# Kernel optimization log

Measured on AMD Instinct MI355X. Metric: run time of the kernel, lower is better.

Reference implementation:

```python
import jax, jax.numpy as jnp
import numpy as np

B, T, D, H = 4, 2048, 512, 8
DH = D // H  # 64
EPS = 1e-5


def setup_inputs() -> dict:
    key = jax.random.key(0)
    ks = jax.random.split(key, 12)
    s = lambda k, shp, fan: jax.random.normal(k, shp, jnp.float32) * (fan ** -0.5)
    return {
        "x": jax.random.normal(ks[0], (B, T, D), jnp.float32),
        "ln1_g": jnp.ones((D,), jnp.float32),
        "ln1_b": jnp.zeros((D,), jnp.float32),
        "Wq": s(ks[1], (H, D, DH), D),  # per-head bias-free projections
        "Wk": s(ks[2], (H, D, DH), D),
        "Wv": s(ks[3], (H, D, DH), D),
        "Wproj": s(ks[4], (D, D), D),
        "bproj": jnp.zeros((D,), jnp.float32),
        "W1": s(ks[5], (D, 4 * D), D),
        "b1": jnp.zeros((4 * D,), jnp.float32),
        "W2": s(ks[6], (4 * D, D), 4 * D),
        "b2": jnp.zeros((D,), jnp.float32),
    }


def _layernorm(x, g, b):
    m = jnp.mean(x, axis=-1, keepdims=True)
    v = jnp.var(x, axis=-1, keepdims=True)
    return (x - m) * jax.lax.rsqrt(v + EPS) * g + b


def reference(x, ln1_g, ln1_b, Wq, Wk, Wv, Wproj, bproj, W1, b1, W2, b2):
    b, t, c = x.shape
    scale = c ** -0.5  # source scales by input channel dim, not head_size
    causal = jnp.tril(jnp.ones((t, t), bool))  # [T,T]

    # --- attention sublayer (pre-norm with ln1) ---
    h = _layernorm(x, ln1_g, ln1_b)
    q = jnp.einsum('btd,hde->bhte', h, Wq)
    k = jnp.einsum('btd,hde->bhte', h, Wk)
    v = jnp.einsum('btd,hde->bhte', h, Wv)
    scores = jnp.einsum('bhte,bhse->bhts', q, k) * scale  # [B,H,T,T]
    scores = jnp.where(causal, scores, -jnp.inf)
    att = jax.nn.softmax(scores, axis=-1)  # dropout = identity at inference
    o = jnp.einsum('bhts,bhse->bthe', att, v).reshape(b, t, c)  # concat heads
    sa = o @ Wproj + bproj
    x = x + sa

    # --- FFN sublayer (source reuses ln1, faithful) ---
    h2 = _layernorm(x, ln1_g, ln1_b)
    ff = jax.nn.relu(h2 @ W1 + b1) @ W2 + b2
    return x + ff
```

## Files before the change

### kernel.cpp

```cpp
#include <hip/hip_runtime.h>
#include <math.h>

#define B_ 4
#define T_ 2048
#define D_ 512
#define H_ 8
#define DH_ 64
#define BT_ 8192
#define FF_ 2048
#define EPS_ 1e-5f
#define SCALE_ 0.04419417382415922f
#define SC2_ 0.06375861151f
#define NEGINF_ -1e30f

typedef short b16x8 __attribute__((ext_vector_type(8)));
typedef short b16x4 __attribute__((ext_vector_type(4)));
typedef float f32x4 __attribute__((ext_vector_type(4)));

#define MFMA16(a, b, c) __builtin_amdgcn_mfma_f32_16x16x32_bf16(a, b, c, 0, 0, 0)
#define MFMA16K16(a, b, c) __builtin_amdgcn_mfma_f32_16x16x16bf16_1k(a, b, c, 0, 0, 0)

#define GLL16(gp, lp) \
    __builtin_amdgcn_global_load_lds((const __attribute__((address_space(1))) void*)(gp), \
                                     (__attribute__((address_space(3))) void*)(lp), 16, 0, 0)

#if __has_builtin(__builtin_amdgcn_exp2f)
#define EXP2F(x) __builtin_amdgcn_exp2f(x)
#else
#define EXP2F(x) exp2f(x)
#endif

static __device__ inline short f2bf(float f) {
    unsigned int u = __builtin_bit_cast(unsigned int, f);
    unsigned int r = (u + 0x7fffu + ((u >> 16) & 1u)) >> 16;
    return (short)r;
}
static __device__ inline short f2bf_trunc(float f) {
    return (short)(__builtin_bit_cast(unsigned int, f) >> 16);
}
static __device__ inline float bf2f(short s) {
    return __builtin_bit_cast(float, ((unsigned int)(unsigned short)s) << 16);
}

__global__ __launch_bounds__(256) void prologue_kernel(
        const float* __restrict__ Wq, const float* __restrict__ Wk,
        const float* __restrict__ Wv, const float* __restrict__ Wp,
        const float* __restrict__ W1, const float* __restrict__ W2,
        short* __restrict__ wqkv, short* __restrict__ wpt,
        short* __restrict__ w1t, short* __restrict__ w2t,
        const float* __restrict__ X, const float* __restrict__ G,
        const float* __restrict__ Bb, short* __restrict__ Y)
{
    __shared__ float tile[32][33];
    int idx = blockIdx.x;
    if (idx >= 3072) {
        int tid = threadIdx.y * 32 + threadIdx.x;
        int wave = tid >> 6, t = tid & 63;
        int row = (idx - 3072) * 4 + wave;
        const float* xr = X + (size_t)row * D_;
        float4 v0 = *(const float4*)(xr + t * 4);
        float4 v1 = *(const float4*)(xr + 256 + t * 4);
        float sum = v0.x + v0.y + v0.z + v0.w + v1.x + v1.y + v1.z + v1.w;
        float ssq = v0.x*v0.x + v0.y*v0.y + v0.z*v0.z + v0.w*v0.w
                  + v1.x*v1.x + v1.y*v1.y + v1.z*v1.z + v1.w*v1.w;
        #pragma unroll
        for (int off = 32; off > 0; off >>= 1) {
            sum += __shfl_down(sum, off);
            ssq += __shfl_down(ssq, off);
        }
        sum = __shfl(sum, 0);
        ssq = __shfl(ssq, 0);
        float mean = sum * (1.0f / D_);
        float var  = ssq * (1.0f / D_) - mean * mean;
        float rstd = rsqrtf(var + EPS_);
        float4 g0 = *(const float4*)(G + t * 4);
        float4 g1 = *(const float4*)(G + 256 + t * 4);
        float4 b0 = *(const float4*)(Bb + t * 4);
        float4 b1 = *(const float4*)(Bb + 256 + t * 4);
        short4 o0, o1;
        o0.x = f2bf((v0.x - mean) * rstd * g0.x + b0.x);
        o0.y = f2bf((v0.y - mean) * rstd * g0.y + b0.y);
        o0.z = f2bf((v0.z - mean) * rstd * g0.z + b0.z);
        o0.w = f2bf((v0.w - mean) * rstd * g0.w + b0.w);
        o1.x = f2bf((v1.x - mean) * rstd * g1.x + b1.x);
        o1.y = f2bf((v1.y - mean) * rstd * g1.y + b1.y);
        o1.z = f2bf((v1.z - mean) * rstd * g1.z + b1.z);
        o1.w = f2bf((v1.w - mean) * rstd * g1.w + b1.w);
        short* yr = Y + (size_t)row * D_;
        *(short4*)(yr + t * 4)       = o0;
        *(short4*)(yr + 256 + t * 4) = o1;
        return;
    }
    const float* src; short* dst; int R, C, tx0, ty0;
    if (idx < 768) {
        int w = idx >> 8, rem = idx & 255;
        int hh = rem >> 5, t = rem & 31;
        const float* base = (w == 0) ? Wq : ((w == 1) ? Wk : Wv);
        src = base + hh * (D_ * DH_);
        dst = wqkv + w * (512 * 512) + hh * (DH_ * D_);
        R = 512; C = 64; tx0 = (t & 1) * 32; ty0 = (t >> 1) * 32;
    } else if (idx < 1024) {
        int t = idx - 768;
        src = Wp; dst = wpt; R = 512; C = 512;
        tx0 = (t & 15) * 32; ty0 = (t >> 4) * 32;
    } else if (idx < 2048) {
        int t = idx - 1024;
        src = W1; dst = w1t; R = 512; C = 2048;
        tx0 = (t & 63) * 32; ty0 = (t >> 6) * 32;
    } else {
        int t = idx - 2048;
        src = W2; dst = w2t; R = 2048; C = 512;
        tx0 = (t & 15) * 32; ty0 = (t >> 4) * 32;
    }
    int tx = threadIdx.x, ty = threadIdx.y;
    #pragma unroll
    for (int i = 0; i < 32; i += 8)
        tile[ty + i][tx] = src[(size_t)(ty0 + ty + i) * C + tx0 + tx];
    __syncthreads();
    #pragma unroll
    for (int i = 0; i < 32; i += 8)
        dst[(size_t)(tx0 + ty + i) * R + ty0 + tx] = f2bf(tile[tx][ty + i]);
}

__global__ __launch_bounds__(256) void ln_bf16_kernel(const short* __restrict__ X,
        const float* __restrict__ G, const float* __restrict__ Bb,
        short* __restrict__ Y)
{
    int wave = threadIdx.x >> 6, t = threadIdx.x & 63;
    int row = blockIdx.x * 4 + wave;
    const short* xr = X + (size_t)row * D_ + t * 8;
    b16x8 xv = *(const b16x8*)xr;
    float v[8];
    float sum = 0.0f, ssq = 0.0f;
    #pragma unroll
    for (int e = 0; e < 8; ++e) {
        v[e] = bf2f(xv[e]);
        sum += v[e];
        ssq += v[e] * v[e];
    }
    #pragma unroll
    for (int off = 32; off > 0; off >>= 1) {
        sum += __shfl_down(sum, off);
        ssq += __shfl_down(ssq, off);
    }
    sum = __shfl(sum, 0);
    ssq = __shfl(ssq, 0);
    float mean = sum * (1.0f / D_);
    float var  = ssq * (1.0f / D_) - mean * mean;
    float rstd = rsqrtf(var + EPS_);

    float4 g0 = *(const float4*)(G + t * 8);
    float4 g1 = *(const float4*)(G + t * 8 + 4);
    float4 b0 = *(const float4*)(Bb + t * 8);
    float4 b1 = *(const float4*)(Bb + t * 8 + 4);
    float gg[8] = {g0.x, g0.y, g0.z, g0.w, g1.x, g1.y, g1.z, g1.w};
    float bb[8] = {b0.x, b0.y, b0.z, b0.w, b1.x, b1.y, b1.z, b1.w};
    b16x8 o;
    #pragma unroll
    for (int e = 0; e < 8; ++e)
        o[e] = f2bf((v[e] - mean) * rstd * gg[e] + bb[e]);
    *(b16x8*)(Y + (size_t)row * D_ + t * 8) = o;
}

__global__ __launch_bounds__(512, 2) void mm256_kernel(const short* __restrict__ A,
        const short* __restrict__ Bt, void* __restrict__ C,
        const float* __restrict__ bias, int relu, int N, int K)
{
    __shared__ short As[2][256 * 64];
    __shared__ short Bs[2][256 * 64];
    const int tid = threadIdx.x;
    const int wave = tid >> 6, lane = tid & 63;
    const int quad = lane >> 4, l15 = lane & 15;
    const int m0 = blockIdx.x * 256, n0 = blockIdx.y * 256;
    const int mw = (wave & 1) * 128, nw = (wave >> 1) * 64;

#define STAGE_M256(bufi, kk) \
    { \
        for (int r = 0; r < 4; ++r) { \
            int c = r * 512 + tid; \
            int row = c >> 3, seg = (c & 7) ^ (row & 7); \
            GLL16(A + (size_t)(m0 + row) * K + (kk) + seg * 8, \
                  As[bufi] + (size_t)(r * 512 + wave * 64) * 8); \
            GLL16(Bt + (size_t)(n0 + row) * K + (kk) + seg * 8, \
                  Bs[bufi] + (size_t)(r * 512 + wave * 64) * 8); \
        } \
    }

    f32x4 acc[8][4];
    #pragma unroll
    for (int i = 0; i < 8; ++i)
        #pragma unroll
        for (int j = 0; j < 4; ++j)
            acc[i][j] = (f32x4){0.f, 0.f, 0.f, 0.f};

    const int NT = K >> 6;
    STAGE_M256(0, 0);
    int buf = 0;
    for (int t = 0; t < NT; ++t) {
        __syncthreads();
        if (t + 1 < NT) STAGE_M256(buf ^ 1, (t + 1) * 64);
        #pragma unroll
        for (int kb = 0; kb < 2; ++kb) {
            b16x8 af[8], bf[4];
            #pragma unroll
            for (int i = 0; i < 8; ++i) {
                int row = mw + i * 16 + l15;
                af[i] = *(const b16x8*)(As[buf] + row * 64 + (((kb * 4 + quad) ^ (row & 7)) * 8));
            }
            #pragma unroll
            for (int j = 0; j < 4; ++j) {
                int row = nw + j * 16 + l15;
                bf[j] = *(const b16x8*)(Bs[buf] + row * 64 + (((kb * 4 + quad) ^ (row & 7)) * 8));
            }
            #pragma unroll
            for (int i = 0; i < 8; ++i)
                #pragma unroll
                for (int j = 0; j < 4; ++j)
                    acc[i][j] = MFMA16(af[i], bf[j], acc[i][j]);
        }
        buf ^= 1;
    }
#undef STAGE_M256

    #pragma unroll
    for (int i = 0; i < 8; ++i) {
        #pragma unroll
        for (int r = 0; r < 4; ++r) {
            size_t row = (size_t)(m0 + mw + i * 16 + quad * 4 + r);
            #pragma unroll
            for (int j = 0; j < 4; ++j) {
                int col = n0 + nw + j * 16 + l15;
                float v = acc[i][j][r];
                if (bias)  v += bias[col];
                if (relu)  v = fmaxf(v, 0.0f);
                ((short*)C)[row * N + col] = f2bf(v);
            }
        }
    }
}

__global__ __launch_bounds__(256) void mm6464_kernel(const short* __restrict__ A,
        const short* __restrict__ Bt, void* __restrict__ C,
        const float* __restrict__ bias, const void* __restrict__ resid,
        int M, int N, int K, int relu, int out_bf16, int resid_bf16)
{
    __shared__ short As[2][64 * 64];
    __shared__ short Bs[2][64 * 64];
    const int tid = threadIdx.x;
    const int wave = tid >> 6, lane = tid & 63;
    const int quad = lane >> 4, l15 = lane & 15;
    const int m0 = blockIdx.x * 64, n0 = blockIdx.y * 64;
    const int nw = wave * 16;

#define STAGE_M66(bufi, kk) \
    { \
        for (int r = 0; r < 2; ++r) { \
            int c = r * 256 + tid; \
            int row = c >> 3, seg = (c & 7) ^ (row & 7); \
            GLL16(A + (size_t)(m0 + row) * K + (kk) + seg * 8, \
                  As[bufi] + (size_t)(r * 256 + wave * 64) * 8); \
            GLL16(Bt + (size_t)(n0 + row) * K + (kk) + seg * 8, \
                  Bs[bufi] + (size_t)(r * 256 + wave * 64) * 8); \
        } \
    }

    f32x4 acc[4];
    #pragma unroll
    for (int i = 0; i < 4; ++i) acc[i] = (f32x4){0.f, 0.f, 0.f, 0.f};

    STAGE_M66(0, 0);
    int buf = 0;
    for (int k0 = 0; k0 < K; k0 += 64) {
        __syncthreads();
        if (k0 + 64 < K) STAGE_M66(buf ^ 1, k0 + 64);
        b16x8 af[4][2], bf[2];
        #pragma unroll
        for (int i = 0; i < 4; ++i)
            #pragma unroll
            for (int kb = 0; kb < 2; ++kb) {
                int row = i * 16 + l15;
                af[i][kb] = *(const b16x8*)(As[buf] + row * 64 + (((kb * 4 + quad) ^ (row & 7)) * 8));
            }
        #pragma unroll
        for (int kb = 0; kb < 2; ++kb) {
            int row = nw + l15;
            bf[kb] = *(const b16x8*)(Bs[buf] + row * 64 + (((kb * 4 + quad) ^ (row & 7)) * 8));
        }
        #pragma unroll
        for (int kb = 0; kb < 2; ++kb)
            #pragma unroll
            for (int i = 0; i < 4; ++i)
                acc[i] = MFMA16(af[i][kb], bf[kb], acc[i]);
        buf ^= 1;
    }
#undef STAGE_M66

    #pragma unroll
    for (int i = 0; i < 4; ++i) {
        #pragma unroll
        for (int r = 0; r < 4; ++r) {
            size_t row = (size_t)(m0 + i * 16 + quad * 4 + r);
            int col = n0 + nw + l15;
            float v = acc[i][r];
            if (bias)  v += bias[col];
            if (resid) {
                if (resid_bf16) v += bf2f(((const short*)resid)[row * N + col]);
                else            v += ((const float*)resid)[row * N + col];
            }
            if (relu)  v = fmaxf(v, 0.0f);
            if (out_bf16) ((short*)C)[row * N + col] = f2bf(v);
            else          ((float*)C)[row * N + col] = v;
        }
    }
}

__global__ __launch_bounds__(256) void attn_kernel(const short* __restrict__ qkv,
        short* __restrict__ Opart, float* __restrict__ Ml)
{
    __shared__ short Qs[64 * 72];
    __shared__ short Ks[64 * 64];
    __shared__ short Vt[64 * 64];

    const int tid = threadIdx.x;
    const int wave = tid >> 6, lane = tid & 63;
    const int quad = lane >> 4, l15 = lane & 15;
    const int bh = blockIdx.x;
    const int qi = 31 - (int)blockIdx.y;
    const int split = blockIdx.z;
    const int b = bh >> 3, h = bh & 7;
    const size_t tok0 = (size_t)b * T_;
    const int qrow_rel = wave * 16 + l15;
    const int half = (qi + 1) >> 1;
    const int klo = split ? half : 0;
    const int khi = split ? qi + 1 : half;
    const int pidx = split * 1024 + bh * 32 + qi;
    short* Op = Opart + (size_t)pidx * 4096;
    float* mlp = Ml + (size_t)pidx * 64;

    if (klo >= khi) {
        for (int i = tid; i < 2048; i += 256) ((int*)Op)[i] = 0;
        if (tid < 64) mlp[tid] = 0.0f;
        return;
    }

    #pragma unroll
    for (int r = 0; r < 2; ++r) {
        int c = r * 256 + tid;
        int tk = c >> 3;
        int seg = (c & 7) ^ (tk & 7);
        GLL16(qkv + (tok0 + qi * 64 + tk) * 1536 + h * 64 + seg * 8,
              Qs + (size_t)(r * 256 + wave * 64) * 8);
    }

    float lrow = 0.0f;
    f32x4 ot[4];
    #pragma unroll
    for (int dt = 0; dt < 4; ++dt) ot[dt] = (f32x4){0.f, 0.f, 0.f, 0.f};

    b16x8 qf[2];

    for (int kj = klo; kj < khi; ++kj) {
        __syncthreads();
        #pragma unroll
        for (int r = 0; r < 2; ++r) {
            int c = r * 256 + tid;
            int tk = c >> 3;
            int seg = (c & 7) ^ (tk & 7);
            GLL16(qkv + (tok0 + kj * 64 + tk) * 1536 + 512 + h * 64 + seg * 8,
                  Ks + (size_t)(r * 256 + wave * 64) * 8);
        }
        {
            int s = tid >> 5, tp = tid & 31;
            const short* g0 = qkv + (tok0 + kj * 64 + tp * 2) * 1536 + 1024 + h * 64 + s * 8;
            b16x8 v0 = *(const b16x8*)g0;
            b16x8 v1 = *(const b16x8*)(g0 + 1536);
            int* vo = (int*)Vt;
            int gg = tp >> 1, hlf = tp & 1;
            #pragma unroll
            for (int e = 0; e < 8; ++e) {
                int row = s * 8 + e;
                unsigned int pk = (unsigned int)(unsigned short)v0[e]
                                | ((unsigned int)(unsigned short)v1[e] << 16);
                vo[row * 32 + ((gg ^ (row & 15)) << 1) + hlf] = pk;
            }
        }
        __syncthreads();

        if (kj == klo) {
            #pragma unroll
            for (int kb = 0; kb < 2; ++kb) {
                int row = wave * 16 + l15;
                qf[kb] = *(const b16x8*)(Qs + row * 64 + (((kb * 4 + quad) ^ (row & 7)) * 8));
            }
        }

        f32x4 st[4];
        #pragma unroll
        for (int mt = 0; mt < 4; ++mt) st[mt] = (f32x4){0.f, 0.f, 0.f, 0.f};
        #pragma unroll
        for (int mt = 0; mt < 4; ++mt) {
            int trow = mt * 16 + l15;
            #pragma unroll
            for (int kb = 0; kb < 2; ++kb) {
                b16x8 kf = *(const b16x8*)(Ks + trow * 64 + (((kb * 4 + quad) ^ (trow & 7)) * 8));
                st[mt] = MFMA16(kf, qf[kb], st[mt]);
            }
        }

        const bool diag = (kj == qi);
        float rs = 0.0f;
        b16x4 pf[4];
        #pragma unroll
        for (int mt = 0; mt < 4; ++mt)
            #pragma unroll
            for (int r = 0; r < 4; ++r) {
                float s = st[mt][r];
                if (diag && (mt * 16 + quad * 4 + r) > qrow_rel) s = NEGINF_;
                float e = EXP2F(s * SC2_);
                rs += e;
                pf[mt][r] = f2bf_trunc(e);
            }
        rs += __shfl_xor(rs, 16);
        rs += __shfl_xor(rs, 32);
        lrow += rs;
        #pragma unroll
        for (int dt = 0; dt < 4; ++dt) {
            const short* vrow = Vt + (dt * 16 + l15) * 64;
            #pragma unroll
            for (int kt = 0; kt < 4; ++kt) {
                b16x4 vf = *(const b16x4*)(vrow + (((kt * 4 + quad) ^ l15) << 2));
                ot[dt] = MFMA16K16(vf, pf[kt], ot[dt]);
            }
        }
    }

    __syncthreads();
    float inv = 1.0f / lrow;
    #pragma unroll
    for (int dt = 0; dt < 4; ++dt) {
        b16x4 o4;
        o4[0] = f2bf(ot[dt][0] * inv);
        o4[1] = f2bf(ot[dt][1] * inv);
        o4[2] = f2bf(ot[dt][2] * inv);
        o4[3] = f2bf(ot[dt][3] * inv);
        *(b16x4*)(Qs + (size_t)qrow_rel * 72 + dt * 16 + quad * 4) = o4;
    }
    {
        int row = tid >> 2, ch = tid & 3;
        b16x8 lo = *(const b16x8*)(Qs + (size_t)row * 72 + ch * 16);
        b16x8 hi = *(const b16x8*)(Qs + (size_t)row * 72 + ch * 16 + 8);
        short* dst = Op + row * 64 + ch * 16;
        *(b16x8*)dst = lo;
        *(b16x8*)(dst + 8) = hi;
    }
    if (quad == 0) mlp[qrow_rel] = lrow;
}

__global__ __launch_bounds__(256) void attn_combine_kernel(
        const short* __restrict__ Opart, const float* __restrict__ Ml,
        short* __restrict__ Ob)
{
    int pair = blockIdx.x;
    int bh = pair >> 5, qi = pair & 31;
    int b = bh >> 3, h = bh & 7;
    int tid = threadIdx.x;
    const short* O1 = Opart + (size_t)pair * 4096;
    const short* O2 = Opart + (size_t)(1024 + pair) * 4096;
    const float* ml1 = Ml + (size_t)pair * 64;
    const float* ml2 = Ml + (size_t)(1024 + pair) * 64;
    int ch = tid & 7;
    #pragma unroll
    for (int it = 0; it < 2; ++it) {
        int row = it * 32 + (tid >> 3);
        float l1 = ml1[row], l2 = ml2[row];
        float inv = 1.0f / (l1 + l2);
        float w1 = l1 * inv, w2 = l2 * inv;
        b16x8 a = *(const b16x8*)(O1 + row * 64 + ch * 8);
        b16x8 c = *(const b16x8*)(O2 + row * 64 + ch * 8);
        b16x8 o;
        #pragma unroll
        for (int e = 0; e < 8; ++e)
            o[e] = f2bf(w1 * bf2f(a[e]) + w2 * bf2f(c[e]));
        short* dst = Ob + ((size_t)(b * T_ + qi * 64 + row)) * 512 + h * 64 + ch * 8;
        *(b16x8*)dst = o;
    }
}

extern "C" void kernel_launch(void* const* d_in, const int* in_sizes, int n_in,
                              void* d_out, int out_size, void* d_ws, size_t ws_size,
                              hipStream_t stream) {
    (void)in_sizes; (void)n_in; (void)out_size; (void)ws_size;
    const float* x     = (const float*)d_in[0];
    const float* ln_g  = (const float*)d_in[1];
    const float* ln_b  = (const float*)d_in[2];
    const float* Wq    = (const float*)d_in[3];
    const float* Wk    = (const float*)d_in[4];
    const float* Wv    = (const float*)d_in[5];
    const float* Wproj = (const float*)d_in[6];
    const float* bproj = (const float*)d_in[7];
    const float* W1    = (const float*)d_in[8];
    const float* b1    = (const float*)d_in[9];
    const float* W2    = (const float*)d_in[10];
    const float* b2    = (const float*)d_in[11];
    float* out = (float*)d_out;

    char* W = (char*)d_ws;
    short* hbuf  = (short*)(W + 0);
    short* qkvb  = (short*)(W + ((size_t)8  << 20));
    short* attno = (short*)(W + ((size_t)32 << 20));
    short* x1b   = (short*)(W + ((size_t)40 << 20));
    short* ff1   = (short*)(W + ((size_t)56 << 20));
    short* wqkv  = (short*)(W + ((size_t)88 << 20));
    short* wpt   = (short*)(W + ((size_t)90 << 20));
    short* w1t   = (short*)(W + ((size_t)91 << 20));
    short* w2t   = (short*)(W + ((size_t)93 << 20));
    short* Opart = (short*)(W + ((size_t)96 << 20));
    float* Ml    = (float*)(W + ((size_t)112 << 20));

    prologue_kernel<<<dim3(3072 + BT_ / 4), dim3(32, 8), 0, stream>>>(
        Wq, Wk, Wv, Wproj, W1, W2, wqkv, wpt, w1t, w2t,
        x, ln_g, ln_b, hbuf);
    mm256_kernel<<<dim3(32, 6), dim3(512), 0, stream>>>(hbuf, wqkv, qkvb,
        nullptr, 0, 1536, D_);
    attn_kernel<<<dim3(32, 32, 2), dim3(256), 0, stream>>>(qkvb, Opart, Ml);
    attn_combine_kernel<<<dim3(1024), dim3(256), 0, stream>>>(Opart, Ml, attno);
    mm6464_kernel<<<dim3(128, 8), dim3(256), 0, stream>>>(attno, wpt, x1b,
        bproj, x, BT_, D_, D_, 0, 1, 0);
    ln_bf16_kernel<<<dim3(BT_ / 4), dim3(256), 0, stream>>>(x1b, ln_g, ln_b, hbuf);
    mm256_kernel<<<dim3(32, 8), dim3(512), 0, stream>>>(hbuf, w1t, ff1,
        b1, 1, FF_, D_);
    mm6464_kernel<<<dim3(128, 8), dim3(256), 0, stream>>>(ff1, w2t, out,
        b2, x1b, BT_, D_, FF_, 0, 0, 1);
}
```

Measured before the change: 251.6 us.

## Enlarge attention query tile to 128 rows to reuse K/V tiles across two query groups

Each attention block now handles 128 query rows instead of 64, with each wave computing two 16-row query groups that share every K and V fragment loaded from LDS. This halves the number of blocks and the K/V global-to-LDS traffic per query row, and the key-range split between the two z-slices is now even per tile, so the empty-split early exit goes away. In exchange it raises register pressure (doubled accumulators), applies the causal mask across two diagonal key tiles, and the combine kernel is adjusted to the new partition layout.

```diff
diff --git a/kernel.cpp b/kernel.cpp
--- a/kernel.cpp
+++ b/kernel.cpp
@@ -317,47 +317,45 @@
 __global__ __launch_bounds__(256) void attn_kernel(const short* __restrict__ qkv,
         short* __restrict__ Opart, float* __restrict__ Ml)
 {
-    __shared__ short Qs[64 * 72];
-    __shared__ short Ks[64 * 64];
-    __shared__ short Vt[64 * 64];
+    __shared__ short smem[16384];
+    short* Qs = smem;
+    short* Ks = smem + 8192;
+    short* Vt = smem + 12288;
 
     const int tid = threadIdx.x;
     const int wave = tid >> 6, lane = tid & 63;
     const int quad = lane >> 4, l15 = lane & 15;
     const int bh = blockIdx.x;
-    const int qi = 31 - (int)blockIdx.y;
+    const int qb = 15 - (int)blockIdx.y;
     const int split = blockIdx.z;
     const int b = bh >> 3, h = bh & 7;
     const size_t tok0 = (size_t)b * T_;
-    const int qrow_rel = wave * 16 + l15;
-    const int half = (qi + 1) >> 1;
+    const int half = qb + 1;
     const int klo = split ? half : 0;
-    const int khi = split ? qi + 1 : half;
-    const int pidx = split * 1024 + bh * 32 + qi;
-    short* Op = Opart + (size_t)pidx * 4096;
-    float* mlp = Ml + (size_t)pidx * 64;
-
-    if (klo >= khi) {
-        for (int i = tid; i < 2048; i += 256) ((int*)Op)[i] = 0;
-        if (tid < 64) mlp[tid] = 0.0f;
-        return;
-    }
-
-    #pragma unroll
-    for (int r = 0; r < 2; ++r) {
+    const int khi = split ? 2 * qb + 2 : half;
+    const int pidx = split * 512 + bh * 16 + qb;
+    short* Op = Opart + (size_t)pidx * 8192;
+    float* mlp = Ml + (size_t)pidx * 128;
+
+    #pragma unroll
+    for (int r = 0; r < 4; ++r) {
         int c = r * 256 + tid;
         int tk = c >> 3;
         int seg = (c & 7) ^ (tk & 7);
-        GLL16(qkv + (tok0 + qi * 64 + tk) * 1536 + h * 64 + seg * 8,
+        GLL16(qkv + (tok0 + qb * 128 + tk) * 1536 + h * 64 + seg * 8,
               Qs + (size_t)(r * 256 + wave * 64) * 8);
     }
 
-    float lrow = 0.0f;
-    f32x4 ot[4];
-    #pragma unroll
-    for (int dt = 0; dt < 4; ++dt) ot[dt] = (f32x4){0.f, 0.f, 0.f, 0.f};
-
-    b16x8 qf[2];
+    float lrow[2] = {0.0f, 0.0f};
+    f32x4 ot[4][2];
+    #pragma unroll
+    for (int dt = 0; dt < 4; ++dt)
+        #pragma unroll
+        for (int qg = 0; qg < 2; ++qg)
+            ot[dt][qg] = (f32x4){0.f, 0.f, 0.f, 0.f};
+
+    b16x8 qf[2][2];
+    const int qrel0 = wave * 32 + l15;
 
     for (int kj = klo; kj < khi; ++kj) {
         __syncthreads();
@@ -388,72 +386,99 @@
 
         if (kj == klo) {
             #pragma unroll
-            for (int kb = 0; kb < 2; ++kb) {
-                int row = wave * 16 + l15;
-                qf[kb] = *(const b16x8*)(Qs + row * 64 + (((kb * 4 + quad) ^ (row & 7)) * 8));
-            }
-        }
-
-        f32x4 st[4];
-        #pragma unroll
-        for (int mt = 0; mt < 4; ++mt) st[mt] = (f32x4){0.f, 0.f, 0.f, 0.f};
+            for (int qg = 0; qg < 2; ++qg)
+                #pragma unroll
+                for (int kb = 0; kb < 2; ++kb) {
+                    int row = qrel0 + qg * 16;
+                    qf[qg][kb] = *(const b16x8*)(Qs + row * 64 + (((kb * 4 + quad) ^ (row & 7)) * 8));
+                }
+        }
+
+        f32x4 st[4][2];
+        #pragma unroll
+        for (int mt = 0; mt < 4; ++mt)
+            #pragma unroll
+            for (int qg = 0; qg < 2; ++qg)
+                st[mt][qg] = (f32x4){0.f, 0.f, 0.f, 0.f};
         #pragma unroll
         for (int mt = 0; mt < 4; ++mt) {
             int trow = mt * 16 + l15;
             #pragma unroll
             for (int kb = 0; kb < 2; ++kb) {
                 b16x8 kf = *(const b16x8*)(Ks + trow * 64 + (((kb * 4 + quad) ^ (trow & 7)) * 8));
-                st[mt] = MFMA16(kf, qf[kb], st[mt]);
-            }
-        }
-
-        const bool diag = (kj == qi);
-        float rs = 0.0f;
-        b16x4 pf[4];
+                #pragma unroll
+                for (int qg = 0; qg < 2; ++qg)
+                    st[mt][qg] = MFMA16(kf, qf[qg][kb], st[mt][qg]);
+            }
+        }
+
+        const bool need_mask = (kj >= 2 * qb);
+        const int moff = kj * 64 - qb * 128;
+        float rs[2] = {0.0f, 0.0f};
+        b16x4 pf[4][2];
         #pragma unroll
         for (int mt = 0; mt < 4; ++mt)
             #pragma unroll
-            for (int r = 0; r < 4; ++r) {
-                float s = st[mt][r];
-                if (diag && (mt * 16 + quad * 4 + r) > qrow_rel) s = NEGINF_;
-                float e = EXP2F(s * SC2_);
-                rs += e;
-                pf[mt][r] = f2bf_trunc(e);
-            }
-        rs += __shfl_xor(rs, 16);
-        rs += __shfl_xor(rs, 32);
-        lrow += rs;
+            for (int qg = 0; qg < 2; ++qg)
+                #pragma unroll
+                for (int r = 0; r < 4; ++r) {
+                    float s = st[mt][qg][r];
+                    if (need_mask && (moff + mt * 16 + quad * 4 + r) > (qrel0 + qg * 16)) s = NEGINF_;
+                    float e = EXP2F(s * SC2_);
+                    rs[qg] += e;
+                    pf[mt][qg][r] = f2bf_trunc(e);
+                }
+        #pragma unroll
+        for (int qg = 0; qg < 2; ++qg) {
+            rs[qg] += __shfl_xor(rs[qg], 16);
+            rs[qg] += __shfl_xor(rs[qg], 32);
+            lrow[qg] += rs[qg];
+        }
+
         #pragma unroll
         for (int dt = 0; dt < 4; ++dt) {
             const short* vrow = Vt + (dt * 16 + l15) * 64;
-            #pragma unroll
-            for (int kt = 0; kt < 4; ++kt) {
-                b16x4 vf = *(const b16x4*)(vrow + (((kt * 4 + quad) ^ l15) << 2));
-                ot[dt] = MFMA16K16(vf, pf[kt], ot[dt]);
-            }
+            b16x4 vf[4];
+            #pragma unroll
+            for (int kt = 0; kt < 4; ++kt)
+                vf[kt] = *(const b16x4*)(vrow + (((kt * 4 + quad) ^ l15) << 2));
+            #pragma unroll
+            for (int qg = 0; qg < 2; ++qg)
+                #pragma unroll
+                for (int kt = 0; kt < 4; ++kt)
+                    ot[dt][qg] = MFMA16K16(vf[kt], pf[kt][qg], ot[dt][qg]);
         }
     }
 
     __syncthreads();
-    float inv = 1.0f / lrow;
-    #pragma unroll
-    for (int dt = 0; dt < 4; ++dt) {
-        b16x4 o4;
-        o4[0] = f2bf(ot[dt][0] * inv);
-        o4[1] = f2bf(ot[dt][1] * inv);
-        o4[2] = f2bf(ot[dt][2] * inv);
-        o4[3] = f2bf(ot[dt][3] * inv);
-        *(b16x4*)(Qs + (size_t)qrow_rel * 72 + dt * 16 + quad * 4) = o4;
+    short* strip = smem;
+    #pragma unroll
+    for (int qg = 0; qg < 2; ++qg) {
+        float inv = (lrow[qg] > 0.0f) ? 1.0f / lrow[qg] : 0.0f;
+        int qr = qrel0 + qg * 16;
+        #pragma unroll
+        for (int dt = 0; dt < 4; ++dt) {
+            b16x4 o4;
+            o4[0] = f2bf(ot[dt][qg][0] * inv);
+            o4[1] = f2bf(ot[dt][qg][1] * inv);
+            o4[2] = f2bf(ot[dt][qg][2] * inv);
+            o4[3] = f2bf(ot[dt][qg][3] * inv);
+            *(b16x4*)(strip + (size_t)qr * 72 + dt * 16 + quad * 4) = o4;
+        }
     }
     {
-        int row = tid >> 2, ch = tid & 3;
-        b16x8 lo = *(const b16x8*)(Qs + (size_t)row * 72 + ch * 16);
-        b16x8 hi = *(const b16x8*)(Qs + (size_t)row * 72 + ch * 16 + 8);
-        short* dst = Op + row * 64 + ch * 16;
-        *(b16x8*)dst = lo;
-        *(b16x8*)(dst + 8) = hi;
-    }
-    if (quad == 0) mlp[qrow_rel] = lrow;
+        int row = tid >> 1, ch = tid & 1;
+        const short* sp = strip + (size_t)row * 72 + ch * 32;
+        short* dst = Op + row * 64 + ch * 32;
+        *(b16x8*)(dst)      = *(const b16x8*)(sp);
+        *(b16x8*)(dst + 8)  = *(const b16x8*)(sp + 8);
+        *(b16x8*)(dst + 16) = *(const b16x8*)(sp + 16);
+        *(b16x8*)(dst + 24) = *(const b16x8*)(sp + 24);
+    }
+    if (quad == 0) {
+        mlp[qrel0]      = lrow[0];
+        mlp[qrel0 + 16] = lrow[1];
+    }
 }
 
 __global__ __launch_bounds__(256) void attn_combine_kernel(
@@ -461,16 +486,16 @@
         short* __restrict__ Ob)
 {
     int pair = blockIdx.x;
-    int bh = pair >> 5, qi = pair & 31;
+    int bh = pair >> 4, qb = pair & 15;
     int b = bh >> 3, h = bh & 7;
     int tid = threadIdx.x;
-    const short* O1 = Opart + (size_t)pair * 4096;
-    const short* O2 = Opart + (size_t)(1024 + pair) * 4096;
-    const float* ml1 = Ml + (size_t)pair * 64;
-    const float* ml2 = Ml + (size_t)(1024 + pair) * 64;
+    const short* O1 = Opart + (size_t)pair * 8192;
+    const short* O2 = Opart + (size_t)(512 + pair) * 8192;
+    const float* ml1 = Ml + (size_t)pair * 128;
+    const float* ml2 = Ml + (size_t)(512 + pair) * 128;
     int ch = tid & 7;
     #pragma unroll
-    for (int it = 0; it < 2; ++it) {
+    for (int it = 0; it < 4; ++it) {
         int row = it * 32 + (tid >> 3);
         float l1 = ml1[row], l2 = ml2[row];
         float inv = 1.0f / (l1 + l2);
@@ -481,7 +506,7 @@
         #pragma unroll
         for (int e = 0; e < 8; ++e)
             o[e] = f2bf(w1 * bf2f(a[e]) + w2 * bf2f(c[e]));
-        short* dst = Ob + ((size_t)(b * T_ + qi * 64 + row)) * 512 + h * 64 + ch * 8;
+        short* dst = Ob + ((size_t)(b * T_ + qb * 128 + row)) * 512 + h * 64 + ch * 8;
         *(b16x8*)dst = o;
     }
 }
@@ -522,8 +547,8 @@
         x, ln_g, ln_b, hbuf);
     mm256_kernel<<<dim3(32, 6), dim3(512), 0, stream>>>(hbuf, wqkv, qkvb,
         nullptr, 0, 1536, D_);
-    attn_kernel<<<dim3(32, 32, 2), dim3(256), 0, stream>>>(qkvb, Opart, Ml);
-    attn_combine_kernel<<<dim3(1024), dim3(256), 0, stream>>>(Opart, Ml, attno);
+    attn_kernel<<<dim3(32, 16, 2), dim3(256), 0, stream>>>(qkvb, Opart, Ml);
+    attn_combine_kernel<<<dim3(512), dim3(256), 0, stream>>>(Opart, Ml, attno);
     mm6464_kernel<<<dim3(128, 8), dim3(256), 0, stream>>>(attno, wpt, x1b,
         bproj, x, BT_, D_, D_, 0, 1, 0);
     ln_bf16_kernel<<<dim3(BT_ / 4), dim3(256), 0, stream>>>(x1b, ln_g, ln_b, hbuf);
```

New measurement: 259.6 us. 3.2% more time.
